# Optimization experiments

Hardware: AMD Instinct MI355X
Metric: run time of the kernel (lower is better)

Reference implementation:

```python
import jax, jax.numpy as jnp
import numpy as np

N_NODES = 100000
N_EDGES = 1000000
D_FEAT = 64
N_GRAPHS = 64


def setup_inputs() -> dict:
    key = jax.random.key(0)
    ks = jax.random.split(key, 5)
    x = jax.random.normal(ks[0], (N_NODES, D_FEAT), dtype=jnp.float32)
    edge_index = jax.random.randint(ks[1], (2, N_EDGES), 0, N_NODES, dtype=jnp.int32)
    batch = jnp.sort(jax.random.randint(ks[2], (N_NODES,), 0, N_GRAPHS, dtype=jnp.int32))
    s = 1.0 / np.sqrt(D_FEAT)
    W1 = jax.random.uniform(ks[3], (D_FEAT, D_FEAT), jnp.float32, -s, s)
    W2 = jax.random.uniform(ks[4], (D_FEAT, D_FEAT), jnp.float32, -s, s)
    b1 = jnp.zeros((D_FEAT,), jnp.float32)
    b2 = jnp.zeros((D_FEAT,), jnp.float32)
    return {"x": x, "edge_index": edge_index, "batch": batch,
            "W1": W1, "b1": b1, "W2": W2, "b2": b2}


def gcn_conv(x, edge_index, W, b, num_nodes):
    # PyG GCNConv: h = D^{-1/2} (A + I) D^{-1/2} (x W) + b
    loops = jnp.arange(num_nodes, dtype=edge_index.dtype)
    row = jnp.concatenate([edge_index[0], loops])  # source nodes
    col = jnp.concatenate([edge_index[1], loops])  # target nodes
    h = x @ W  # [N, D]
    deg = jax.ops.segment_sum(jnp.ones_like(col, dtype=h.dtype), col,
                              num_segments=num_nodes)  # >= 1 due to self loops
    dinv = jax.lax.rsqrt(deg)
    norm = dinv[row] * dinv[col]  # [E+N]
    out = jax.ops.segment_sum(h[row] * norm[:, None], col, num_segments=num_nodes)
    return out + b


def reference(x, edge_index, batch, W1, b1, W2, b2):
    n = x.shape[0]
    h = gcn_conv(x, edge_index, W1, b1, n)
    h = gcn_conv(h, edge_index, W2, b2, n)
    # global_mean_pool over graph ids
    sums = jax.ops.segment_sum(h, batch, num_segments=N_GRAPHS)  # [G, D]
    cnts = jax.ops.segment_sum(jnp.ones((n, 1), h.dtype), batch,
                               num_segments=N_GRAPHS)
    return sums / jnp.maximum(cnts, 1.0)
```

## Files before the change

### kernel.cpp

```cpp
#include <hip/hip_runtime.h>
#include <hip/hip_fp16.h>

#define DFEAT 64
#define NG 64
#define TILE 128
#define NBLK 256
#define NBMAX 1024
#define NREP 16

__global__ __launch_bounds__(256) void k_cnt(const int* __restrict__ col,
                                             int* __restrict__ cnt_m,
                                             int e, int nb, int chunk) {
  __shared__ int hist[NBMAX];
  int tid = threadIdx.x;
  int blk = blockIdx.x;
  for (int b = tid; b < nb; b += 256) hist[b] = 0;
  __syncthreads();
  int lo = blk * chunk, hi = min(lo + chunk, e);
  for (int i = lo + tid; i < hi; i += 256)
    atomicAdd(&hist[col[i] >> 7], 1);
  __syncthreads();
  for (int b = tid; b < nb; b += 256)
    cnt_m[(size_t)blk * nb + b] = hist[b];
}

__global__ __launch_bounds__(256) void k_colscan(int* __restrict__ cnt_m,
                                                 int* __restrict__ gcount, int nb) {
  __shared__ int sh[256];
  int tid = threadIdx.x;
  int b = blockIdx.x;
  int v = cnt_m[(size_t)tid * nb + b];
  sh[tid] = v;
  __syncthreads();
  for (int off = 1; off < 256; off <<= 1) {
    int t = (tid >= off) ? sh[tid - off] : 0;
    __syncthreads();
    sh[tid] += t;
    __syncthreads();
  }
  cnt_m[(size_t)tid * nb + b] = sh[tid] - v;
  if (tid == 255) gcount[b] = sh[255];
}

__global__ __launch_bounds__(1024) void k_bscan(const int* __restrict__ gcount,
                                                int* __restrict__ base, int nb) {
  __shared__ int sh[1024];
  int tid = threadIdx.x;
  int v = (tid < nb) ? gcount[tid] : 0;
  sh[tid] = v;
  __syncthreads();
  for (int off = 1; off < 1024; off <<= 1) {
    int t = (tid >= off) ? sh[tid - off] : 0;
    __syncthreads();
    sh[tid] += t;
    __syncthreads();
  }
  if (tid < nb) base[tid] = sh[tid] - v;
  if (tid == 0) base[nb] = sh[1023];
}

__global__ __launch_bounds__(256) void k_bin2(const int* __restrict__ row,
                                              const int* __restrict__ col,
                                              const int* __restrict__ base,
                                              const int* __restrict__ cnt_m,
                                              int* __restrict__ pairs,
                                              int e, int nb, int chunk) {
  __shared__ int gl[NBMAX];
  __shared__ int lcur[NBMAX];
  int tid = threadIdx.x;
  int blk = blockIdx.x;
  for (int b = tid; b < nb; b += 256) {
    gl[b] = base[b] + cnt_m[(size_t)blk * nb + b];
    lcur[b] = 0;
  }
  __syncthreads();
  int lo = blk * chunk, hi = min(lo + chunk, e);
  for (int i = lo + tid; i < hi; i += 256) {
    int s = row[i], t = col[i];
    int b = t >> 7;
    int pos = gl[b] + atomicAdd(&lcur[b], 1);
    pairs[pos] = s | ((t & (TILE - 1)) << 20);
  }
}

__global__ __launch_bounds__(256) void k_csr(const int* __restrict__ pairs,
                                             const int* __restrict__ base,
                                             const float* __restrict__ x,
                                             int* __restrict__ starts,
                                             int* __restrict__ srcs,
                                             float* __restrict__ dinv,
                                             __half2* __restrict__ xh,
                                             int n, int e) {
  __shared__ int cnt[TILE];
  __shared__ int cur[TILE];
  __shared__ int sc[TILE];
  __shared__ float sdv[TILE];
  int tid = threadIdx.x;
  int b = blockIdx.x;
  int tile0 = b * TILE;
  if (tid < TILE) cnt[tid] = 0;
  __syncthreads();
  int e0 = base[b], e1 = base[b + 1];
  for (int i = e0 + tid; i < e1; i += 256)
    atomicAdd(&cnt[(unsigned)pairs[i] >> 20], 1);
  __syncthreads();
  int c = (tid < TILE) ? cnt[tid] : 0;
  if (tid < TILE) sc[tid] = c;
  __syncthreads();
  for (int off = 1; off < TILE; off <<= 1) {
    int t = (tid < TILE && tid >= off) ? sc[tid - off] : 0;
    __syncthreads();
    if (tid < TILE) sc[tid] += t;
    __syncthreads();
  }
  if (tid < TILE) {
    int excl = sc[tid] - c;
    cur[tid] = excl;
    int node = tile0 + tid;
    float d = rsqrtf(1.0f + (float)c);
    sdv[tid] = (node < n) ? d : 0.f;
    if (node < n) {
      starts[node] = e0 + excl;
      dinv[node] = d;
    }
  }
  if (b == 0 && tid == 0) starts[n] = e;
  __syncthreads();
  for (int i = e0 + tid; i < e1; i += 256) {
    int p = pairs[i];
    int pos = atomicAdd(&cur[(unsigned)p >> 20], 1);
    srcs[e0 + pos] = p & 0xFFFFF;
  }
  int nnode = min(n - tile0, TILE);
  if (nnode > 0) {
    int nfl = nnode * 16;
    const float4* xf = (const float4*)(x + (size_t)tile0 * 64);
    float2* xo = (float2*)xh + (size_t)tile0 * 16;
    for (int p = tid; p < nfl; p += 256) {
      float4 v = xf[p];
      float d = sdv[p >> 4];
      float2 st;
      ((__half2*)&st)[0] = __floats2half2_rn(v.x * d, v.y * d);
      ((__half2*)&st)[1] = __floats2half2_rn(v.z * d, v.w * d);
      xo[p] = st;
    }
  }
}

__global__ __launch_bounds__(256) void k_w12(const float* __restrict__ W1,
                                             const float* __restrict__ W2,
                                             const float* __restrict__ b1,
                                             const int* __restrict__ batch,
                                             float* __restrict__ WW,
                                             float* __restrict__ bw,
                                             float* __restrict__ cntf, int n) {
  __shared__ float w1[4096], w2[4096];
  int tid = threadIdx.x;
  for (int i = tid; i < 4096; i += 256) { w1[i] = W1[i]; w2[i] = W2[i]; }
  if (tid < NG) {
    int g = tid;
    int lo = 0, hi = n;
    while (lo < hi) { int m = (lo + hi) >> 1; if (batch[m] < g) lo = m + 1; else hi = m; }
    int a = lo;
    lo = 0; hi = n;
    while (lo < hi) { int m = (lo + hi) >> 1; if (batch[m] < g + 1) lo = m + 1; else hi = m; }
    cntf[g] = (float)(lo - a);
  }
  __syncthreads();
  for (int p = tid; p < 4096; p += 256) {
    int k = p >> 6, d = p & 63;
    float a = 0.f;
    for (int m = 0; m < 64; ++m) a += w1[k * 64 + m] * w2[m * 64 + d];
    WW[p] = a;
  }
  if (tid < 64) {
    float a = 0.f;
    for (int k = 0; k < 64; ++k) a += b1[k] * w2[k * 64 + tid];
    bw[tid] = a;
  }
}

__device__ __forceinline__ void acc8w(float2& a0, float2& a1, float2& a2,
                                      float2& a3, float4 v, float w) {
  const __half2* hp = (const __half2*)&v;
  float2 t;
  t = __half22float2(hp[0]); a0.x = fmaf(w, t.x, a0.x); a0.y = fmaf(w, t.y, a0.y);
  t = __half22float2(hp[1]); a1.x = fmaf(w, t.x, a1.x); a1.y = fmaf(w, t.y, a1.y);
  t = __half22float2(hp[2]); a2.x = fmaf(w, t.x, a2.x); a2.y = fmaf(w, t.y, a2.y);
  t = __half22float2(hp[3]); a3.x = fmaf(w, t.x, a3.x); a3.y = fmaf(w, t.y, a3.y);
}
__device__ __forceinline__ void acc8(float2& a0, float2& a1, float2& a2,
                                     float2& a3, float4 v) {
  const __half2* hp = (const __half2*)&v;
  float2 t;
  t = __half22float2(hp[0]); a0.x += t.x; a0.y += t.y;
  t = __half22float2(hp[1]); a1.x += t.x; a1.y += t.y;
  t = __half22float2(hp[2]); a2.x += t.x; a2.y += t.y;
  t = __half22float2(hp[3]); a3.x += t.x; a3.y += t.y;
}

__global__ __launch_bounds__(256) void k_gather1(const int* __restrict__ starts,
                                                 const int* __restrict__ srcs,
                                                 const float* __restrict__ dinv,
                                                 const __half2* __restrict__ xh,
                                                 const int* __restrict__ batch,
                                                 __half2* __restrict__ z1h,
                                                 float* __restrict__ Tr, int n) {
  int tid = threadIdx.x;
  int node = blockIdx.x * 32 + (tid >> 3);
  bool act = node < n;
  int nc = act ? node : n - 1;
  int l = tid & 7;
  int lane = tid & 63;
  int rep = blockIdx.x & (NREP - 1);
  int s = starts[nc];
  int deg = act ? (starts[nc + 1] - s) : 0;
  float dc = dinv[nc];
  int g = batch[nc];
  const float4* xf = (const float4*)xh;
  float4 sv = xf[(size_t)nc * 8 + l];
  float2 a0 = make_float2(0.f, 0.f), a1 = a0, a2 = a0, a3 = a0;
  acc8(a0, a1, a2, a3, sv);
  float wsum = 0.f;
  int trips = (deg + 7) >> 3;
  int dm1 = deg - 1;
  int r[8];
  if (trips > 0) {
#pragma unroll
    for (int k = 0; k < 8; ++k) r[k] = srcs[s + min(k, dm1)];
  }
  int j = 0;
  for (int t = 0; t < trips; ++t) {
    int cur[8];
#pragma unroll
    for (int k = 0; k < 8; ++k) cur[k] = r[k];
    int jn = j + 8;
#pragma unroll
    for (int k = 0; k < 8; ++k) r[k] = srcs[s + min(jn + k, dm1)];
    float4 v[8];
#pragma unroll
    for (int k = 0; k < 8; ++k) v[k] = xf[(size_t)cur[k] * 8 + l];
    float dv[8];
#pragma unroll
    for (int k = 0; k < 8; ++k) dv[k] = dinv[cur[k]];
    float w[8];
#pragma unroll
    for (int k = 0; k < 8; ++k) w[k] = (j + k < deg) ? 1.f : 0.f;
#pragma unroll
    for (int k = 0; k < 8; ++k) wsum = fmaf(w[k], dv[k], wsum);
#pragma unroll
    for (int k = 0; k < 8; ++k) acc8w(a0, a1, a2, a3, v[k], w[k]);
    j = jn;
  }
  if (act) {
    float s2 = dc * dc;
    float4 ov;
    __half2* op = (__half2*)&ov;
    op[0] = __floats2half2_rn(s2 * a0.x, s2 * a0.y);
    op[1] = __floats2half2_rn(s2 * a1.x, s2 * a1.y);
    op[2] = __floats2half2_rn(s2 * a2.x, s2 * a2.y);
    op[3] = __floats2half2_rn(s2 * a3.x, s2 * a3.y);
    ((float4*)z1h)[(size_t)node * 8 + l] = ov;
  }
  float uval = act ? dc * (dc + wsum) : 0.f;
  int g0 = __shfl(g, 0);
  bool uni = (__all(g == g0) != 0);
  if (!uni) {
    if (act && l == 0) unsafeAtomicAdd(&Tr[rep * NG + g], uval);
  } else {
    float uv = (l == 0) ? uval : 0.f;
    uv += __shfl_xor(uv, 8);
    uv += __shfl_xor(uv, 16);
    uv += __shfl_xor(uv, 32);
    if (lane == 0 && uv != 0.f) unsafeAtomicAdd(&Tr[rep * NG + g0], uv);
  }
}

__global__ __launch_bounds__(256) void k_gather2(const int* __restrict__ starts,
                                                 const int* __restrict__ srcs,
                                                 const float* __restrict__ dinv,
                                                 const __half2* __restrict__ z1h,
                                                 const int* __restrict__ batch,
                                                 float* __restrict__ Pb,
                                                 float* __restrict__ S, int n) {
  __shared__ float rowacc[2][64];
  __shared__ int sgid[2];
  int tid = threadIdx.x;
  int blk0 = (int)blockIdx.x * 32;
  int node = blk0 + (tid >> 3);
  bool act = node < n;
  int nc = act ? node : n - 1;
  int l = tid & 7;
  int lane = tid & 63;
  int s = starts[nc];
  int deg = act ? (starts[nc + 1] - s) : 0;
  float dc = dinv[nc];
  int g = batch[nc];
  if (tid < 128) ((float*)rowacc)[tid] = 0.f;
  if (tid < 2) {
    int idx = blk0 + (tid ? 31 : 0);
    if (idx > n - 1) idx = n - 1;
    sgid[tid] = batch[idx];
  }
  const float4* xf = (const float4*)z1h;
  float4 sv = xf[(size_t)nc * 8 + l];
  float2 a0 = make_float2(0.f, 0.f), a1 = a0, a2 = a0, a3 = a0;
  acc8(a0, a1, a2, a3, sv);
  int trips = (deg + 7) >> 3;
  int dm1 = deg - 1;
  int r[8];
  if (trips > 0) {
#pragma unroll
    for (int k = 0; k < 8; ++k) r[k] = srcs[s + min(k, dm1)];
  }
  int j = 0;
  for (int t = 0; t < trips; ++t) {
    int cur[8];
#pragma unroll
    for (int k = 0; k < 8; ++k) cur[k] = r[k];
    int jn = j + 8;
#pragma unroll
    for (int k = 0; k < 8; ++k) r[k] = srcs[s + min(jn + k, dm1)];
    float4 v[8];
#pragma unroll
    for (int k = 0; k < 8; ++k) v[k] = xf[(size_t)cur[k] * 8 + l];
    float w[8];
#pragma unroll
    for (int k = 0; k < 8; ++k) w[k] = (j + k < deg) ? 1.f : 0.f;
#pragma unroll
    for (int k = 0; k < 8; ++k) acc8w(a0, a1, a2, a3, v[k], w[k]);
    j = jn;
  }
  float f[8];
  f[0] = act ? dc * a0.x : 0.f;
  f[1] = act ? dc * a0.y : 0.f;
  f[2] = act ? dc * a1.x : 0.f;
  f[3] = act ? dc * a1.y : 0.f;
  f[4] = act ? dc * a2.x : 0.f;
  f[5] = act ? dc * a2.y : 0.f;
  f[6] = act ? dc * a3.x : 0.f;
  f[7] = act ? dc * a3.y : 0.f;
  __syncthreads();
  int g_lo = sgid[0], g_hi = sgid[1];
  int sel = (g == g_lo) ? 0 : ((g == g_hi) ? 1 : -1);
  if (sel < 0 && act) {
#pragma unroll
    for (int k = 0; k < 8; ++k)
      unsafeAtomicAdd(&S[g * 64 + l * 8 + k], f[k]);
  }
  float fa[8], fb[8];
#pragma unroll
  for (int k = 0; k < 8; ++k) {
    fa[k] = (sel == 0) ? f[k] : 0.f;
    fb[k] = (sel == 1) ? f[k] : 0.f;
  }
#pragma unroll
  for (int k = 0; k < 8; ++k) {
    fa[k] += __shfl_xor(fa[k], 8);
    fa[k] += __shfl_xor(fa[k], 16);
    fa[k] += __shfl_xor(fa[k], 32);
    fb[k] += __shfl_xor(fb[k], 8);
    fb[k] += __shfl_xor(fb[k], 16);
    fb[k] += __shfl_xor(fb[k], 32);
  }
  if (lane < 8) {
#pragma unroll
    for (int k = 0; k < 8; ++k) {
      if (fa[k] != 0.f) atomicAdd(&rowacc[0][lane * 8 + k], fa[k]);
      if (fb[k] != 0.f) atomicAdd(&rowacc[1][lane * 8 + k], fb[k]);
    }
  }
  __syncthreads();
  float* pb = Pb + (size_t)blockIdx.x * 130;
  if (tid < 128) pb[tid] = ((float*)rowacc)[tid];
  if (tid == 128) pb[128] = (float)g_lo;
  if (tid == 129) pb[129] = (float)g_hi;
}

__global__ __launch_bounds__(256) void k_sreduce(const float* __restrict__ Pb,
                                                 const int* __restrict__ batch,
                                                 float* __restrict__ S, int n) {
  __shared__ float sh[4][64];
  int g = blockIdx.x;
  int d = threadIdx.x & 63, r = threadIdx.x >> 6;
  int lo = 0, hi = n;
  while (lo < hi) { int m = (lo + hi) >> 1; if (batch[m] < g) lo = m + 1; else hi = m; }
  int a = lo;
  lo = 0; hi = n;
  while (lo < hi) { int m = (lo + hi) >> 1; if (batch[m] < g + 1) lo = m + 1; else hi = m; }
  int b = lo;
  float acc = 0.f;
  if (b > a) {
    int bl0 = a >> 5, bl1 = (b - 1) >> 5;
    for (int bl = bl0 + r; bl <= bl1; bl += 4) {
      const float* p = Pb + (size_t)bl * 130;
      if ((int)p[128] == g) acc += p[d];
      if ((int)p[129] == g) acc += p[64 + d];
    }
  }
  sh[r][d] = acc;
  __syncthreads();
  if (r == 0) S[g * 64 + d] += acc + sh[1][d] + sh[2][d] + sh[3][d];
}

__global__ __launch_bounds__(256) void k_final2(const float* __restrict__ S,
                                                const float* __restrict__ Tr,
                                                const float* __restrict__ cntf,
                                                const float* __restrict__ WW,
                                                const float* __restrict__ bw,
                                                const float* __restrict__ b2,
                                                float* __restrict__ out) {
  __shared__ float sS[4096], sW[4096], sT[64];
  int tid = threadIdx.x;
  for (int i = tid; i < 4096; i += 256) {
    sS[i] = S[i];
    sW[i] = WW[i];
  }
  if (tid < 64) {
    float t = 0.f;
    for (int r = 0; r < NREP; ++r) t += Tr[r * NG + tid];
    sT[tid] = t;
  }
  __syncthreads();
  for (int p = tid; p < 4096; p += 256) {
    int g = p >> 6, d = p & 63;
    float a = 0.f;
    for (int k = 0; k < 64; ++k) a += sS[g * 64 + k] * sW[k * 64 + d];
    float c = fmaxf(cntf[g], 1.0f);
    out[p] = (a + sT[g] * bw[d]) / c + b2[d];
  }
}

extern "C" void kernel_launch(void* const* d_in, const int* in_sizes, int n_in,
                              void* d_out, int out_size, void* d_ws, size_t ws_size,
                              hipStream_t stream) {
  const float* x = (const float*)d_in[0];
  const int* ei = (const int*)d_in[1];
  const int* bat = (const int*)d_in[2];
  const float* W1 = (const float*)d_in[3];
  const float* b1 = (const float*)d_in[4];
  const float* W2 = (const float*)d_in[5];
  const float* b2 = (const float*)d_in[6];
  float* out = (float*)d_out;

  int n = in_sizes[0] / 64;
  int e = in_sizes[1] / 2;
  const int* rowp = ei;
  const int* colp = ei + e;
  int nb = (n + TILE - 1) / TILE;
  int chunk = (e + NBLK - 1) / NBLK;
  int nbw = (n + 31) / 32;

  char* ws = (char*)d_ws;
  size_t off = 0;
  auto alloc = [&](size_t elems) {
    void* p = ws + off;
    off += ((elems * 4 + 255) & ~(size_t)255);
    return p;
  };
  float* S = (float*)alloc(NG * DFEAT);
  float* Tr = (float*)alloc(NREP * NG);
  float* cntf = (float*)alloc(NG);
  size_t zbytes = off;
  int* gcount = (int*)alloc(nb);
  int* base = (int*)alloc(nb + 1);
  int* cnt_m = (int*)alloc((size_t)NBLK * nb);
  float* dinv = (float*)alloc(n);
  int* starts = (int*)alloc(n + 1);
  int* srcs = (int*)alloc(e);
  float* WW = (float*)alloc(DFEAT * DFEAT);
  float* bw = (float*)alloc(DFEAT);
  __half2* xh = (__half2*)alloc((size_t)n * 32);
  __half2* z1h = (__half2*)alloc((size_t)n * 32);
  int* pairs = (int*)alloc(e);
  float* Pb = (float*)alloc((size_t)nbw * 130);

  (void)hipMemsetAsync(S, 0, zbytes, stream);
  k_cnt<<<NBLK, 256, 0, stream>>>(colp, cnt_m, e, nb, chunk);
  k_colscan<<<nb, 256, 0, stream>>>(cnt_m, gcount, nb);
  k_bscan<<<1, 1024, 0, stream>>>(gcount, base, nb);
  k_bin2<<<NBLK, 256, 0, stream>>>(rowp, colp, base, cnt_m, pairs, e, nb, chunk);
  k_csr<<<nb, 256, 0, stream>>>(pairs, base, x, starts, srcs, dinv, xh, n, e);
  k_w12<<<1, 256, 0, stream>>>(W1, W2, b1, bat, WW, bw, cntf, n);

  k_gather1<<<nbw, 256, 0, stream>>>(starts, srcs, dinv, xh, bat, z1h, Tr, n);
  k_gather2<<<nbw, 256, 0, stream>>>(starts, srcs, dinv, z1h, bat, Pb, S, n);
  k_sreduce<<<NG, 256, 0, stream>>>(Pb, bat, S, n);

  k_final2<<<1, 256, 0, stream>>>(S, Tr, cntf, WW, bw, b2, out);
}
```

Measured before the change: 212.8 us.

## Replace second-layer pull gather with source-binned push into per-tile graph sums

```diff
diff --git a/kernel.cpp b/kernel.cpp
--- a/kernel.cpp
+++ b/kernel.cpp
@@ -8,28 +8,40 @@
 #define NBMAX 1024
 #define NREP 16
 
-__global__ __launch_bounds__(256) void k_cnt(const int* __restrict__ col,
+__global__ __launch_bounds__(256) void k_cnt(const int* __restrict__ row,
+                                             const int* __restrict__ col,
                                              int* __restrict__ cnt_m,
+                                             int* __restrict__ cnt_m2,
                                              int e, int nb, int chunk) {
-  __shared__ int hist[NBMAX];
+  __shared__ int hist[NBMAX], hist2[NBMAX];
   int tid = threadIdx.x;
   int blk = blockIdx.x;
-  for (int b = tid; b < nb; b += 256) hist[b] = 0;
+  for (int b = tid; b < nb; b += 256) { hist[b] = 0; hist2[b] = 0; }
   __syncthreads();
   int lo = blk * chunk, hi = min(lo + chunk, e);
-  for (int i = lo + tid; i < hi; i += 256)
+  for (int i = lo + tid; i < hi; i += 256) {
     atomicAdd(&hist[col[i] >> 7], 1);
-  __syncthreads();
-  for (int b = tid; b < nb; b += 256)
+    atomicAdd(&hist2[row[i] >> 7], 1);
+  }
+  __syncthreads();
+  for (int b = tid; b < nb; b += 256) {
     cnt_m[(size_t)blk * nb + b] = hist[b];
+    cnt_m2[(size_t)blk * nb + b] = hist2[b];
+  }
 }
 
 __global__ __launch_bounds__(256) void k_colscan(int* __restrict__ cnt_m,
-                                                 int* __restrict__ gcount, int nb) {
+                                                 int* __restrict__ cnt_m2,
+                                                 int* __restrict__ gcount,
+                                                 int* __restrict__ gcount2,
+                                                 int nb) {
   __shared__ int sh[256];
   int tid = threadIdx.x;
-  int b = blockIdx.x;
-  int v = cnt_m[(size_t)tid * nb + b];
+  int side = (int)blockIdx.x >= nb;
+  int b = (int)blockIdx.x - (side ? nb : 0);
+  int* m = side ? cnt_m2 : cnt_m;
+  int* gc = side ? gcount2 : gcount;
+  int v = m[(size_t)tid * nb + b];
   sh[tid] = v;
   __syncthreads();
   for (int off = 1; off < 256; off <<= 1) {
@@ -38,15 +50,19 @@
     sh[tid] += t;
     __syncthreads();
   }
-  cnt_m[(size_t)tid * nb + b] = sh[tid] - v;
-  if (tid == 255) gcount[b] = sh[255];
+  m[(size_t)tid * nb + b] = sh[tid] - v;
+  if (tid == 255) gc[b] = sh[255];
 }
 
 __global__ __launch_bounds__(1024) void k_bscan(const int* __restrict__ gcount,
-                                                int* __restrict__ base, int nb) {
+                                                const int* __restrict__ gcount2,
+                                                int* __restrict__ base,
+                                                int* __restrict__ base2, int nb) {
   __shared__ int sh[1024];
   int tid = threadIdx.x;
-  int v = (tid < nb) ? gcount[tid] : 0;
+  const int* gc = blockIdx.x ? gcount2 : gcount;
+  int* bs = blockIdx.x ? base2 : base;
+  int v = (tid < nb) ? gc[tid] : 0;
   sh[tid] = v;
   __syncthreads();
   for (int off = 1; off < 1024; off <<= 1) {
@@ -55,40 +71,49 @@
     sh[tid] += t;
     __syncthreads();
   }
-  if (tid < nb) base[tid] = sh[tid] - v;
-  if (tid == 0) base[nb] = sh[1023];
+  if (tid < nb) bs[tid] = sh[tid] - v;
+  if (tid == 0) bs[nb] = sh[1023];
 }
 
 __global__ __launch_bounds__(256) void k_bin2(const int* __restrict__ row,
                                               const int* __restrict__ col,
                                               const int* __restrict__ base,
+                                              const int* __restrict__ base2,
                                               const int* __restrict__ cnt_m,
+                                              const int* __restrict__ cnt_m2,
                                               int* __restrict__ pairs,
+                                              int* __restrict__ pairs2,
                                               int e, int nb, int chunk) {
-  __shared__ int gl[NBMAX];
-  __shared__ int lcur[NBMAX];
+  __shared__ int gl[NBMAX], lcur[NBMAX], gl2[NBMAX], lcur2[NBMAX];
   int tid = threadIdx.x;
   int blk = blockIdx.x;
   for (int b = tid; b < nb; b += 256) {
     gl[b] = base[b] + cnt_m[(size_t)blk * nb + b];
     lcur[b] = 0;
+    gl2[b] = base2[b] + cnt_m2[(size_t)blk * nb + b];
+    lcur2[b] = 0;
   }
   __syncthreads();
   int lo = blk * chunk, hi = min(lo + chunk, e);
   for (int i = lo + tid; i < hi; i += 256) {
     int s = row[i], t = col[i];
-    int b = t >> 7;
-    int pos = gl[b] + atomicAdd(&lcur[b], 1);
+    int b1 = t >> 7;
+    int pos = gl[b1] + atomicAdd(&lcur[b1], 1);
     pairs[pos] = s | ((t & (TILE - 1)) << 20);
+    int b2 = s >> 7;
+    int pos2 = gl2[b2] + atomicAdd(&lcur2[b2], 1);
+    pairs2[pos2] = t | ((s & (TILE - 1)) << 20);
   }
 }
 
 __global__ __launch_bounds__(256) void k_csr(const int* __restrict__ pairs,
                                              const int* __restrict__ base,
                                              const float* __restrict__ x,
+                                             const int* __restrict__ batch,
                                              int* __restrict__ starts,
                                              int* __restrict__ srcs,
                                              float* __restrict__ dinv,
+                                             float2* __restrict__ tinfo,
                                              __half2* __restrict__ xh,
                                              int n, int e) {
   __shared__ int cnt[TILE];
@@ -122,6 +147,7 @@
     if (node < n) {
       starts[node] = e0 + excl;
       dinv[node] = d;
+      tinfo[node] = make_float2(d, __int_as_float(batch[node]));
     }
   }
   if (b == 0 && tid == 0) starts[n] = e;
@@ -276,131 +302,68 @@
   }
 }
 
-__global__ __launch_bounds__(256) void k_gather2(const int* __restrict__ starts,
-                                                 const int* __restrict__ srcs,
-                                                 const float* __restrict__ dinv,
-                                                 const __half2* __restrict__ z1h,
-                                                 const int* __restrict__ batch,
-                                                 float* __restrict__ Pb,
-                                                 float* __restrict__ S, int n) {
-  __shared__ float rowacc[2][64];
-  __shared__ int sgid[2];
-  int tid = threadIdx.x;
-  int blk0 = (int)blockIdx.x * 32;
-  int node = blk0 + (tid >> 3);
-  bool act = node < n;
-  int nc = act ? node : n - 1;
+__device__ __forceinline__ void pushrow(const unsigned* srow, float* acc,
+                                        int row, int l, float w, int g) {
+  uint4 q = *(const uint4*)&srow[row * 36 + l * 4];
+  float2 f0 = __half22float2(*(const __half2*)&q.x);
+  float2 f1 = __half22float2(*(const __half2*)&q.y);
+  float2 f2 = __half22float2(*(const __half2*)&q.z);
+  float2 f3 = __half22float2(*(const __half2*)&q.w);
+  float* ap = acc + g * 65 + l * 8;
+  atomicAdd(ap + 0, w * f0.x);
+  atomicAdd(ap + 1, w * f0.y);
+  atomicAdd(ap + 2, w * f1.x);
+  atomicAdd(ap + 3, w * f1.y);
+  atomicAdd(ap + 4, w * f2.x);
+  atomicAdd(ap + 5, w * f2.y);
+  atomicAdd(ap + 6, w * f3.x);
+  atomicAdd(ap + 7, w * f3.y);
+}
+
+__global__ __launch_bounds__(256) void k_push2(const int* __restrict__ pairs2,
+                                               const int* __restrict__ base2,
+                                               const float2* __restrict__ tinfo,
+                                               const __half2* __restrict__ z1h,
+                                               float* __restrict__ Sp, int n) {
+  __shared__ float acc[64 * 65];
+  __shared__ unsigned srow[TILE * 36];
+  int tid = threadIdx.x;
+  int b = blockIdx.x;
+  int tile0 = b * TILE;
+  int nnode = min(n - tile0, TILE);
+  for (int i = tid; i < 64 * 65; i += 256) acc[i] = 0.f;
+  const unsigned* zr = (const unsigned*)z1h + (size_t)tile0 * 32;
+  for (int p = tid; p < nnode * 32; p += 256)
+    srow[(p >> 5) * 36 + (p & 31)] = zr[p];
+  __syncthreads();
   int l = tid & 7;
-  int lane = tid & 63;
-  int s = starts[nc];
-  int deg = act ? (starts[nc + 1] - s) : 0;
-  float dc = dinv[nc];
-  int g = batch[nc];
-  if (tid < 128) ((float*)rowacc)[tid] = 0.f;
-  if (tid < 2) {
-    int idx = blk0 + (tid ? 31 : 0);
-    if (idx > n - 1) idx = n - 1;
-    sgid[tid] = batch[idx];
-  }
-  const float4* xf = (const float4*)z1h;
-  float4 sv = xf[(size_t)nc * 8 + l];
-  float2 a0 = make_float2(0.f, 0.f), a1 = a0, a2 = a0, a3 = a0;
-  acc8(a0, a1, a2, a3, sv);
-  int trips = (deg + 7) >> 3;
-  int dm1 = deg - 1;
-  int r[8];
-  if (trips > 0) {
-#pragma unroll
-    for (int k = 0; k < 8; ++k) r[k] = srcs[s + min(k, dm1)];
-  }
-  int j = 0;
-  for (int t = 0; t < trips; ++t) {
-    int cur[8];
-#pragma unroll
-    for (int k = 0; k < 8; ++k) cur[k] = r[k];
-    int jn = j + 8;
-#pragma unroll
-    for (int k = 0; k < 8; ++k) r[k] = srcs[s + min(jn + k, dm1)];
-    float4 v[8];
-#pragma unroll
-    for (int k = 0; k < 8; ++k) v[k] = xf[(size_t)cur[k] * 8 + l];
-    float w[8];
-#pragma unroll
-    for (int k = 0; k < 8; ++k) w[k] = (j + k < deg) ? 1.f : 0.f;
-#pragma unroll
-    for (int k = 0; k < 8; ++k) acc8w(a0, a1, a2, a3, v[k], w[k]);
-    j = jn;
-  }
-  float f[8];
-  f[0] = act ? dc * a0.x : 0.f;
-  f[1] = act ? dc * a0.y : 0.f;
-  f[2] = act ? dc * a1.x : 0.f;
-  f[3] = act ? dc * a1.y : 0.f;
-  f[4] = act ? dc * a2.x : 0.f;
-  f[5] = act ? dc * a2.y : 0.f;
-  f[6] = act ? dc * a3.x : 0.f;
-  f[7] = act ? dc * a3.y : 0.f;
-  __syncthreads();
-  int g_lo = sgid[0], g_hi = sgid[1];
-  int sel = (g == g_lo) ? 0 : ((g == g_hi) ? 1 : -1);
-  if (sel < 0 && act) {
-#pragma unroll
-    for (int k = 0; k < 8; ++k)
-      unsafeAtomicAdd(&S[g * 64 + l * 8 + k], f[k]);
-  }
-  float fa[8], fb[8];
-#pragma unroll
-  for (int k = 0; k < 8; ++k) {
-    fa[k] = (sel == 0) ? f[k] : 0.f;
-    fb[k] = (sel == 1) ? f[k] : 0.f;
-  }
-#pragma unroll
-  for (int k = 0; k < 8; ++k) {
-    fa[k] += __shfl_xor(fa[k], 8);
-    fa[k] += __shfl_xor(fa[k], 16);
-    fa[k] += __shfl_xor(fa[k], 32);
-    fb[k] += __shfl_xor(fb[k], 8);
-    fb[k] += __shfl_xor(fb[k], 16);
-    fb[k] += __shfl_xor(fb[k], 32);
-  }
-  if (lane < 8) {
-#pragma unroll
-    for (int k = 0; k < 8; ++k) {
-      if (fa[k] != 0.f) atomicAdd(&rowacc[0][lane * 8 + k], fa[k]);
-      if (fb[k] != 0.f) atomicAdd(&rowacc[1][lane * 8 + k], fb[k]);
-    }
-  }
-  __syncthreads();
-  float* pb = Pb + (size_t)blockIdx.x * 130;
-  if (tid < 128) pb[tid] = ((float*)rowacc)[tid];
-  if (tid == 128) pb[128] = (float)g_lo;
-  if (tid == 129) pb[129] = (float)g_hi;
-}
-
-__global__ __launch_bounds__(256) void k_sreduce(const float* __restrict__ Pb,
-                                                 const int* __restrict__ batch,
-                                                 float* __restrict__ S, int n) {
+  int grp = tid >> 3;
+  for (int u = grp; u < nnode; u += 32) {
+    float2 ti = tinfo[tile0 + u];
+    pushrow(srow, acc, u, l, ti.x, __float_as_int(ti.y));
+  }
+  int e0 = base2[b], e1 = base2[b + 1];
+  for (int e = e0 + grp; e < e1; e += 32) {
+    int p = pairs2[e];
+    float2 ti = tinfo[p & 0xFFFFF];
+    pushrow(srow, acc, (int)((unsigned)p >> 20), l, ti.x, __float_as_int(ti.y));
+  }
+  __syncthreads();
+  float* sp = Sp + (size_t)b * 4096;
+  for (int i = tid; i < 4096; i += 256) sp[i] = acc[(i >> 6) * 65 + (i & 63)];
+}
+
+__global__ __launch_bounds__(256) void k_sred2(const float* __restrict__ Sp,
+                                               float* __restrict__ S, int nbkt) {
   __shared__ float sh[4][64];
   int g = blockIdx.x;
   int d = threadIdx.x & 63, r = threadIdx.x >> 6;
-  int lo = 0, hi = n;
-  while (lo < hi) { int m = (lo + hi) >> 1; if (batch[m] < g) lo = m + 1; else hi = m; }
-  int a = lo;
-  lo = 0; hi = n;
-  while (lo < hi) { int m = (lo + hi) >> 1; if (batch[m] < g + 1) lo = m + 1; else hi = m; }
-  int b = lo;
   float acc = 0.f;
-  if (b > a) {
-    int bl0 = a >> 5, bl1 = (b - 1) >> 5;
-    for (int bl = bl0 + r; bl <= bl1; bl += 4) {
-      const float* p = Pb + (size_t)bl * 130;
-      if ((int)p[128] == g) acc += p[d];
-      if ((int)p[129] == g) acc += p[64 + d];
-    }
-  }
+  for (int bl = r; bl < nbkt; bl += 4)
+    acc += Sp[(size_t)bl * 4096 + g * 64 + d];
   sh[r][d] = acc;
   __syncthreads();
-  if (r == 0) S[g * 64 + d] += acc + sh[1][d] + sh[2][d] + sh[3][d];
+  if (r == 0) S[g * 64 + d] = acc + sh[1][d] + sh[2][d] + sh[3][d];
 }
 
 __global__ __launch_bounds__(256) void k_final2(const float* __restrict__ S,
@@ -463,29 +426,37 @@
   float* cntf = (float*)alloc(NG);
   size_t zbytes = off;
   int* gcount = (int*)alloc(nb);
+  int* gcount2 = (int*)alloc(nb);
   int* base = (int*)alloc(nb + 1);
-  int* cnt_m = (int*)alloc((size_t)NBLK * nb);
+  int* base2 = (int*)alloc(nb + 1);
   float* dinv = (float*)alloc(n);
   int* starts = (int*)alloc(n + 1);
-  int* srcs = (int*)alloc(e);
   float* WW = (float*)alloc(DFEAT * DFEAT);
   float* bw = (float*)alloc(DFEAT);
+  float2* tinfo = (float2*)alloc((size_t)n * 2);
+  __half2* z1h = (__half2*)alloc((size_t)n * 32);
+  int* pairs2 = (int*)alloc(e);
+  size_t scratch0 = off;
   __half2* xh = (__half2*)alloc((size_t)n * 32);
-  __half2* z1h = (__half2*)alloc((size_t)n * 32);
+  int* srcs = (int*)alloc(e);
   int* pairs = (int*)alloc(e);
-  float* Pb = (float*)alloc((size_t)nbw * 130);
+  int* cnt_m = (int*)alloc((size_t)NBLK * nb);
+  int* cnt_m2 = (int*)alloc((size_t)NBLK * nb);
+  float* Sp = (float*)(ws + scratch0);
 
   (void)hipMemsetAsync(S, 0, zbytes, stream);
-  k_cnt<<<NBLK, 256, 0, stream>>>(colp, cnt_m, e, nb, chunk);
-  k_colscan<<<nb, 256, 0, stream>>>(cnt_m, gcount, nb);
-  k_bscan<<<1, 1024, 0, stream>>>(gcount, base, nb);
-  k_bin2<<<NBLK, 256, 0, stream>>>(rowp, colp, base, cnt_m, pairs, e, nb, chunk);
-  k_csr<<<nb, 256, 0, stream>>>(pairs, base, x, starts, srcs, dinv, xh, n, e);
+  k_cnt<<<NBLK, 256, 0, stream>>>(rowp, colp, cnt_m, cnt_m2, e, nb, chunk);
+  k_colscan<<<2 * nb, 256, 0, stream>>>(cnt_m, cnt_m2, gcount, gcount2, nb);
+  k_bscan<<<2, 1024, 0, stream>>>(gcount, gcount2, base, base2, nb);
+  k_bin2<<<NBLK, 256, 0, stream>>>(rowp, colp, base, base2, cnt_m, cnt_m2,
+                                   pairs, pairs2, e, nb, chunk);
+  k_csr<<<nb, 256, 0, stream>>>(pairs, base, x, bat, starts, srcs, dinv, tinfo,
+                                xh, n, e);
   k_w12<<<1, 256, 0, stream>>>(W1, W2, b1, bat, WW, bw, cntf, n);
 
   k_gather1<<<nbw, 256, 0, stream>>>(starts, srcs, dinv, xh, bat, z1h, Tr, n);
-  k_gather2<<<nbw, 256, 0, stream>>>(starts, srcs, dinv, z1h, bat, Pb, S, n);
-  k_sreduce<<<NG, 256, 0, stream>>>(Pb, bat, S, n);
+  k_push2<<<nb, 256, 0, stream>>>(pairs2, base2, tinfo, z1h, Sp, n);
+  k_sred2<<<NG, 256, 0, stream>>>(Sp, S, nb);
 
   k_final2<<<1, 256, 0, stream>>>(S, Tr, cntf, WW, bw, b2, out);
 }
```

New measurement: 705.5 us. 3.31x slower.
